# Kernel tuning notes

Measured on AMD Instinct MI355X. Metric: run time of the kernel, lower is better.

Reference implementation:

```python
import jax, jax.numpy as jnp
import numpy as np

HID = 128
NUM_LAYERS = 3
B = 256
ND, ED, SD = 16384, 65536, 131072
NP_, EP, SP = 131072, 524288, 524288


def setup_inputs():
    key = jax.random.key(0)
    ks = jax.random.split(key, 40)
    r = lambda i, sh: jax.random.normal(ks[i], sh, jnp.float32) * 0.05
    ri = lambda i, sh, hi: jax.random.randint(ks[i], sh, 0, hi, jnp.int32)
    return {
        'drug_x': r(0, (ND, 78)),
        'prot_x': r(1, (NP_, 70)),
        'd_feature': r(2, (B, HID)),
        'p_feature': r(3, (B, HID)),
        'drug_edge_index': ri(4, (2, ED), ND),
        'drug_batch': jnp.sort(ri(5, (ND,), B)),
        'drug_sub_node': ri(6, (SD,), ND),
        'drug_sub_ind': ri(7, (SD,), ND),
        'prot_edge_index': ri(8, (2, EP), NP_),
        'prot_batch': jnp.sort(ri(9, (NP_,), B)),
        'prot_sub_node': ri(10, (SP,), NP_),
        'prot_sub_ind': ri(11, (SP,), NP_),
        'enc_Wd': r(12, (78, HID)), 'enc_bd': r(13, (HID,)),
        'enc_Wp': r(14, (70, HID)), 'enc_bp': r(15, (HID,)),
        'convW_d': r(16, (NUM_LAYERS, HID, HID)), 'convb_d': r(17, (NUM_LAYERS, HID)),
        'convW_p': r(18, (NUM_LAYERS, HID, HID)), 'convb_p': r(19, (NUM_LAYERS, HID)),
        'bng_d': jnp.ones((NUM_LAYERS, HID), jnp.float32), 'bnb_d': jnp.zeros((NUM_LAYERS, HID), jnp.float32),
        'bng_p': jnp.ones((NUM_LAYERS, HID), jnp.float32), 'bnb_p': jnp.zeros((NUM_LAYERS, HID), jnp.float32),
        'vn_emb_d': r(20, (HID,)), 'vn_emb_p': r(21, (HID,)),
        'vnW_d': r(22, (NUM_LAYERS - 1, HID, HID)), 'vnb_d': r(23, (NUM_LAYERS - 1, HID)),
        'vnW_p': r(24, (NUM_LAYERS - 1, HID, HID)), 'vnb_p': r(25, (NUM_LAYERS - 1, HID)),
        'mlpd1_W': r(26, (2 * HID, HID)), 'mlpd1_b': r(27, (HID,)),
        'mlpd1_g': jnp.ones((HID,), jnp.float32), 'mlpd1_be': jnp.zeros((HID,), jnp.float32),
        'mlpp1_W': r(28, (2 * HID, HID)), 'mlpp1_b': r(29, (HID,)),
        'mlpp1_g': jnp.ones((HID,), jnp.float32), 'mlpp1_be': jnp.zeros((HID,), jnp.float32),
    }


def _bn(x, g, b):
    # training-mode batch norm (batch statistics)
    m = jnp.mean(x, 0)
    v = jnp.var(x, 0)
    return (x - m) * jax.lax.rsqrt(v + 1e-5) * g + b


def _seg_mean(x, ids, n):
    s = jax.ops.segment_sum(x, ids, num_segments=n)
    c = jax.ops.segment_sum(jnp.ones((x.shape[0],), x.dtype), ids, num_segments=n)
    return s / jnp.maximum(c, 1.0)[:, None]


def _gcn(h, W, b, ei, n):
    # PyG GCNConv: sym-normalized A+I, then linear
    src, dst = ei[0], ei[1]
    hw = h @ W
    deg = jax.ops.segment_sum(jnp.ones((src.shape[0],), h.dtype), dst, num_segments=n) + 1.0
    nrm = jax.lax.rsqrt(deg)
    msg = hw[src] * (nrm[src] * nrm[dst])[:, None]  # [E, HID]
    return jax.ops.segment_sum(msg, dst, num_segments=n) + hw * (nrm * nrm)[:, None] + b


def _forward(fl, ints):
    (drug_x, prot_x, d_feature, p_feature, enc_Wd, enc_bd, enc_Wp, enc_bp,
     convW_d, convb_d, convW_p, convb_p, bng_d, bnb_d, bng_p, bnb_p,
     vn_emb_d, vn_emb_p, vnW_d, vnb_d, vnW_p, vnb_p,
     mlpd1_W, mlpd1_b, mlpd1_g, mlpd1_be, mlpp1_W, mlpp1_b, mlpp1_g, mlpp1_be) = fl
    (d_ei, d_batch, d_sn, d_si, p_ei, p_batch, p_sn, p_si) = ints
    Nd, Npn = drug_x.shape[0], prot_x.shape[0]
    Bn = d_feature.shape[0]
    hd = drug_x @ enc_Wd + enc_bd
    hp = prot_x @ enc_Wp + enc_bp
    # virtual node init: learned embedding + pretrained fingerprint feature
    vx_d = vn_emb_d[None, :] + d_feature  # [B, HID]
    vx_p = vn_emb_p[None, :] + p_feature
    for i in range(NUM_LAYERS):
        # virtual-node broadcast -> GCN -> BN -> ReLU (dropout off / eval)
        hd = _gcn(hd + vx_d[d_batch], convW_d[i], convb_d[i], d_ei, Nd)
        hp = _gcn(hp + vx_p[p_batch], convW_p[i], convb_p[i], p_ei, Npn)
        hd = jax.nn.relu(_bn(hd, bng_d[i], bnb_d[i]))
        hp = jax.nn.relu(_bn(hp, bng_p[i], bnb_p[i]))
        # k-hop subgraph structure extraction (scatter_mean back to nodes)
        hd_struct = _seg_mean(hd[d_sn], d_si, Nd)
        hp_struct = _seg_mean(hp[p_sn], p_si, Npn)
        if i < NUM_LAYERS - 1:
            vx_d = vx_d + jax.nn.relu((jax.ops.segment_sum(hd_struct, d_batch, num_segments=Bn) + vx_d) @ vnW_d[i] + vnb_d[i])
            vx_p = vx_p + jax.nn.relu((jax.ops.segment_sum(hp_struct, p_batch, num_segments=Bn) + vx_p) @ vnW_p[i] + vnb_p[i])
    # cross-modal sync: broadcast pooled drug info onto protein nodes & vice versa
    sync_drug = hp_struct + _seg_mean(hd_struct, d_batch, Bn)[p_batch]  # [Np, HID]
    sync_prot = hd_struct + _seg_mean(hp_struct, p_batch, Bn)[d_batch]  # [Nd, HID]
    final_drug = _bn(jnp.concatenate([_seg_mean(sync_prot, d_batch, Bn), d_feature], 1) @ mlpd1_W + mlpd1_b, mlpd1_g, mlpd1_be)
    final_prot = _bn(jnp.concatenate([_seg_mean(sync_drug, p_batch, Bn), p_feature], 1) @ mlpp1_W + mlpp1_b, mlpp1_g, mlpp1_be)
    return final_drug, final_prot


def reference(drug_x, prot_x, d_feature, p_feature, drug_edge_index, drug_batch,
              drug_sub_node, drug_sub_ind, prot_edge_index, prot_batch,
              prot_sub_node, prot_sub_ind, enc_Wd, enc_bd, enc_Wp, enc_bp,
              convW_d, convb_d, convW_p, convb_p, bng_d, bnb_d, bng_p, bnb_p,
              vn_emb_d, vn_emb_p, vnW_d, vnb_d, vnW_p, vnb_p,
              mlpd1_W, mlpd1_b, mlpd1_g, mlpd1_be, mlpp1_W, mlpp1_b, mlpp1_g, mlpp1_be):
    fl = (drug_x, prot_x, d_feature, p_feature, enc_Wd, enc_bd, enc_Wp, enc_bp,
          convW_d, convb_d, convW_p, convb_p, bng_d, bnb_d, bng_p, bnb_p,
          vn_emb_d, vn_emb_p, vnW_d, vnb_d, vnW_p, vnb_p,
          mlpd1_W, mlpd1_b, mlpd1_g, mlpd1_be, mlpp1_W, mlpp1_b, mlpp1_g, mlpp1_be)
    ints = (drug_edge_index, drug_batch, drug_sub_node, drug_sub_ind,
            prot_edge_index, prot_batch, prot_sub_node, prot_sub_ind)
    return _forward(fl, ints)
```

## Files before the change

### kernel.cpp

```cpp
#include <hip/hip_runtime.h>
#include <cstdint>
#include <cstddef>

#define HID 128
#define HB 1024
#define XB 2048

using bf16x8 = __attribute__((ext_vector_type(8))) short;
using f32x4v = __attribute__((ext_vector_type(4))) float;

static __device__ __forceinline__ unsigned short f2b(float x) {
  unsigned int u = __float_as_uint(x);
  unsigned int r = u + 0x7FFFu + ((u >> 16) & 1u);
  return (unsigned short)(r >> 16);
}
static __device__ __forceinline__ float b2f(unsigned short h) {
  return __uint_as_float(((unsigned int)h) << 16);
}

static __device__ __forceinline__ int lowerb(const int* __restrict__ a, int n, int v) {
  int lo = 0, hi = n;
  while (lo < hi) { int m = (lo + hi) >> 1; if (a[m] < v) lo = m + 1; else hi = m; }
  return lo;
}

__global__ __launch_bounds__(256)
void k_prep1(const int* p_dst, int EP, int* deg_p, const int* d_dst, int ED, int* deg_d,
             const int* p_si, int SP, int* scnt_p, const int* d_si, int SD, int* scnt_d,
             const float* Xd, int Kd, unsigned short* Dhi, unsigned short* Dlo, int totD,
             const float* Xp, int Kp, unsigned short* Phi, unsigned short* Plo, int totP,
             const float* convW_d, const float* convW_p,
             const float* enc_Wd, const float* enc_Wp,
             unsigned short* WhiAll, unsigned short* WloAll,
             const float* emb_d, const float* d_feat, float* vx_d,
             const float* emb_p, const float* p_feat, float* vx_p, int vhalf) {
  const int b = blockIdx.x;
  const int tid = threadIdx.x;
  if (b < 4 * HB) {
    const int seg = b & 3, lb = b >> 2;
    const int stride = HB * 256;
    const int* idx = seg == 0 ? p_dst : seg == 1 ? d_dst : seg == 2 ? p_si : d_si;
    int* cnt = seg == 0 ? deg_p : seg == 1 ? deg_d : seg == 2 ? scnt_p : scnt_d;
    const int n = seg == 0 ? EP : seg == 1 ? ED : seg == 2 ? SP : SD;
    for (int i = lb * 256 + tid; i < n; i += stride) atomicAdd(&cnt[idx[i]], 1);
  } else if (b < 4 * HB + XB) {
    const int lb = b - 4 * HB;
    for (int i = lb * 256 + tid; i < totD + totP; i += XB * 256) {
      if (i < totD) {
        const int node = i >> 7, k = i & 127;
        const float v = (k < Kd) ? Xd[(size_t)node * Kd + k] : 0.f;
        const unsigned short hi = f2b(v);
        Dhi[i] = hi;
        Dlo[i] = f2b(v - b2f(hi));
      } else {
        const int j = i - totD;
        const int node = j >> 7, k = j & 127;
        const float v = (k < Kp) ? Xp[(size_t)node * Kp + k] : 0.f;
        const unsigned short hi = f2b(v);
        Phi[j] = hi;
        Plo[j] = f2b(v - b2f(hi));
      }
    }
  } else if (b < 4 * HB + XB + 256) {
    const int lb = b - (4 * HB + XB);
    const int seg = lb >> 5;
    const float* W;
    int K;
    if (seg < 3) { W = convW_d + (size_t)seg * HID * HID; K = 128; }
    else if (seg < 6) { W = convW_p + (size_t)(seg - 3) * HID * HID; K = 128; }
    else if (seg == 6) { W = enc_Wd; K = 78; }
    else { W = enc_Wp; K = 70; }
    unsigned short* Whi = WhiAll + (size_t)seg * HID * HID;
    unsigned short* Wlo = WloAll + (size_t)seg * HID * HID;
    for (int i = (lb & 31) * 256 + tid; i < HID * HID; i += 32 * 256) {
      const int c = i >> 7, k = i & 127;
      const float v = (k < K) ? W[k * HID + c] : 0.f;
      const unsigned short hi = f2b(v);
      Whi[i] = hi;
      Wlo[i] = f2b(v - b2f(hi));
    }
  } else {
    const int lb = b - (4 * HB + XB + 256);
    for (int i = lb * 256 + tid; i < 2 * vhalf; i += 128 * 256) {
      if (i < vhalf) vx_d[i] = emb_d[i & (HID - 1)] + d_feat[i];
      else { const int j = i - vhalf; vx_p[j] = emb_p[j & (HID - 1)] + p_feat[j]; }
    }
  }
}

__global__ void k_nrm_nb(const int* deg_d, float* nrm_d, int ND,
                         const int* deg_p, float* nrm_p, int NP,
                         const int* d_batch, float* nb_d,
                         const int* p_batch, float* nb_p, int B) {
  const int stride = gridDim.x * blockDim.x;
  const int total = ND + NP + 2 * B;
  for (int i = blockIdx.x * blockDim.x + threadIdx.x; i < total; i += stride) {
    if (i < ND) nrm_d[i] = rsqrtf((float)deg_d[i] + 1.0f);
    else if (i < ND + NP) { const int j = i - ND; nrm_p[j] = rsqrtf((float)deg_p[j] + 1.0f); }
    else if (i < ND + NP + B) {
      const int b = i - ND - NP;
      nb_d[b] = (float)(lowerb(d_batch, ND, b + 1) - lowerb(d_batch, ND, b));
    } else {
      const int b = i - ND - NP - B;
      nb_p[b] = (float)(lowerb(p_batch, NP, b + 1) - lowerb(p_batch, NP, b));
    }
  }
}

__global__ __launch_bounds__(256)
void k_scan1_all(const int* c0, int* r0, int n0, int nb0,
                 const int* c1, int* r1, int n1, int nb1,
                 const int* c2, int* r2, int n2, int nb2,
                 const int* c3, int* r3, int n3, int nb3, int* aux) {
  __shared__ int sh[256];
  int b = blockIdx.x, seg = 0;
  if (b >= nb0) { b -= nb0; seg = 1; }
  if (seg == 1 && b >= nb1) { b -= nb1; seg = 2; }
  if (seg == 2 && b >= nb2) { b -= nb2; seg = 3; }
  const int* cnt = seg == 0 ? c0 : seg == 1 ? c1 : seg == 2 ? c2 : c3;
  int* row = seg == 0 ? r0 : seg == 1 ? r1 : seg == 2 ? r2 : r3;
  const int n = seg == 0 ? n0 : seg == 1 ? n1 : seg == 2 ? n2 : n3;
  const int tid = threadIdx.x;
  const int base = b * 1024 + tid * 4;
  int v0 = base + 0 < n ? cnt[base + 0] : 0;
  int v1 = base + 1 < n ? cnt[base + 1] : 0;
  int v2 = base + 2 < n ? cnt[base + 2] : 0;
  int v3 = base + 3 < n ? cnt[base + 3] : 0;
  const int s = v0 + v1 + v2 + v3;
  sh[tid] = s;
  __syncthreads();
  for (int o = 1; o < 256; o <<= 1) {
    const int t = (tid >= o) ? sh[tid - o] : 0;
    __syncthreads();
    sh[tid] += t;
    __syncthreads();
  }
  int excl = sh[tid] - s;
  if (tid == 255) aux[seg * 256 + b] = sh[255];
  if (base + 0 < n) row[base + 0] = excl; excl += v0;
  if (base + 1 < n) row[base + 1] = excl; excl += v1;
  if (base + 2 < n) row[base + 2] = excl; excl += v2;
  if (base + 3 < n) row[base + 3] = excl;
}

__global__ __launch_bounds__(256)
void k_scan2_all(int* aux, int nb0, int nb1, int nb2, int nb3) {
  __shared__ int sh[256];
  const int seg = blockIdx.x;
  const int nb = seg == 0 ? nb0 : seg == 1 ? nb1 : seg == 2 ? nb2 : nb3;
  int* a = aux + seg * 256;
  const int tid = threadIdx.x;
  const int v = tid < nb ? a[tid] : 0;
  sh[tid] = v;
  __syncthreads();
  for (int o = 1; o < 256; o <<= 1) {
    const int t = (tid >= o) ? sh[tid - o] : 0;
    __syncthreads();
    sh[tid] += t;
    __syncthreads();
  }
  if (tid < nb) a[tid] = sh[tid] - v;
}

__global__ __launch_bounds__(256)
void k_scan3_all(int* r0, int n0, int nb0, int t0, int* r1, int n1, int nb1, int t1,
                 int* r2, int n2, int nb2, int t2, int* r3, int n3, int nb3, int t3,
                 const int* aux) {
  int b = blockIdx.x, seg = 0;
  if (b >= nb0) { b -= nb0; seg = 1; }
  if (seg == 1 && b >= nb1) { b -= nb1; seg = 2; }
  if (seg == 2 && b >= nb2) { b -= nb2; seg = 3; }
  int* row = seg == 0 ? r0 : seg == 1 ? r1 : seg == 2 ? r2 : r3;
  const int n = seg == 0 ? n0 : seg == 1 ? n1 : seg == 2 ? n2 : n3;
  const int total = seg == 0 ? t0 : seg == 1 ? t1 : seg == 2 ? t2 : t3;
  const int add = aux[seg * 256 + b];
  const int base = b * 1024 + threadIdx.x * 4;
  #pragma unroll
  for (int k = 0; k < 4; ++k)
    if (base + k < n) row[base + k] += add;
  if (b == 0 && threadIdx.x == 0) row[n] = total;
}

__global__ void k_fill_all(const int* p_src, const int* p_dst, const int* rowE_p, int* curE_p,
                           int* colE_p, int EP,
                           const int* d_src, const int* d_dst, const int* rowE_d, int* curE_d,
                           int* colE_d, int ED,
                           const int* p_sn, const int* p_si, const int* rowS_p, int* curS_p,
                           int* colS_p, int SP,
                           const int* d_sn, const int* d_si, const int* rowS_d, int* curS_d,
                           int* colS_d, int SD) {
  const int seg = blockIdx.x & 3;
  const int lb = blockIdx.x >> 2;
  const int stride = (gridDim.x >> 2) * blockDim.x;
  const int start = lb * blockDim.x + threadIdx.x;
  if (seg == 0) {
    for (int e = start; e < EP; e += stride) {
      const int d = p_dst[e];
      colE_p[rowE_p[d] + atomicAdd(&curE_p[d], 1)] = p_src[e];
    }
  } else if (seg == 1) {
    for (int e = start; e < ED; e += stride) {
      const int d = d_dst[e];
      colE_d[rowE_d[d] + atomicAdd(&curE_d[d], 1)] = d_src[e];
    }
  } else if (seg == 2) {
    for (int j = start; j < SP; j += stride) {
      const int t = p_si[j];
      colS_p[rowS_p[t] + atomicAdd(&curS_p[t], 1)] = p_sn[j];
    }
  } else {
    for (int j = start; j < SD; j += stride) {
      const int t = d_si[j];
      colS_d[rowS_d[t] + atomicAdd(&curS_d[t], 1)] = d_sn[j];
    }
  }
}

template<bool ENC>
__global__ __launch_bounds__(256, 2)
void k_gemm_both(const unsigned short* __restrict__ Zhi0, const unsigned short* __restrict__ Zlo0,
                 const unsigned short* __restrict__ Whi0, const unsigned short* __restrict__ Wlo0,
                 const float* __restrict__ bias0, float* __restrict__ G0, int nbk0,
                 const unsigned short* __restrict__ Zhi1, const unsigned short* __restrict__ Zlo1,
                 const unsigned short* __restrict__ Whi1, const unsigned short* __restrict__ Wlo1,
                 const float* __restrict__ bias1, float* __restrict__ G1,
                 float* __restrict__ stats_sl) {
  __shared__ unsigned short Bt[128 * 132];
  __shared__ float lstats[256];
  const int bid = blockIdx.x;
  const bool isP = bid >= nbk0;
  const int lb = isP ? bid - nbk0 : bid;
  const unsigned short* Zhi = isP ? Zhi1 : Zhi0;
  const unsigned short* Zlo = isP ? Zlo1 : Zlo0;
  const unsigned short* Wthi = isP ? Whi1 : Whi0;
  const unsigned short* Wtlo = isP ? Wlo1 : Wlo0;
  const float* bias = isP ? bias1 : bias0;
  float* G = isP ? G1 : G0;

  const int tid = threadIdx.x;
  const int w = tid >> 6;
  const int l = tid & 63;
  const int l15 = l & 15;
  const int kb = l >> 4;

  for (int i = tid; i < 128 * 16; i += 256) {
    const int c = i >> 4, k8 = i & 15;
    *(bf16x8*)(&Bt[c * 132 + k8 * 8]) = *(const bf16x8*)(Wthi + (size_t)c * 128 + k8 * 8);
  }
  if constexpr (!ENC) lstats[tid] = 0.f;

  const int rbase = lb * 128 + w * 32 + l15;
  bf16x8 ahi[2][4], alo[2][4];
  #pragma unroll
  for (int rt = 0; rt < 2; ++rt)
    #pragma unroll
    for (int ks = 0; ks < 4; ++ks) {
      ahi[rt][ks] = *(const bf16x8*)(Zhi + (size_t)(rbase + rt * 16) * 128 + ks * 32 + kb * 8);
      alo[rt][ks] = *(const bf16x8*)(Zlo + (size_t)(rbase + rt * 16) * 128 + ks * 32 + kb * 8);
    }

  f32x4v acc[2][8];
  #pragma unroll
  for (int rt = 0; rt < 2; ++rt)
    #pragma unroll
    for (int ct = 0; ct < 8; ++ct)
      acc[rt][ct] = (f32x4v){0.f, 0.f, 0.f, 0.f};

  __syncthreads();
  #pragma unroll
  for (int ks = 0; ks < 4; ++ks) {
    #pragma unroll
    for (int ct = 0; ct < 8; ++ct) {
      const bf16x8 b = *(const bf16x8*)(&Bt[(ct * 16 + l15) * 132 + ks * 32 + kb * 8]);
      acc[0][ct] = __builtin_amdgcn_mfma_f32_16x16x32_bf16(ahi[0][ks], b, acc[0][ct], 0, 0, 0);
      acc[1][ct] = __builtin_amdgcn_mfma_f32_16x16x32_bf16(ahi[1][ks], b, acc[1][ct], 0, 0, 0);
      acc[0][ct] = __builtin_amdgcn_mfma_f32_16x16x32_bf16(alo[0][ks], b, acc[0][ct], 0, 0, 0);
      acc[1][ct] = __builtin_amdgcn_mfma_f32_16x16x32_bf16(alo[1][ks], b, acc[1][ct], 0, 0, 0);
    }
  }
  __syncthreads();

  for (int i = tid; i < 128 * 16; i += 256) {
    const int c = i >> 4, k8 = i & 15;
    *(bf16x8*)(&Bt[c * 132 + k8 * 8]) = *(const bf16x8*)(Wtlo + (size_t)c * 128 + k8 * 8);
  }
  __syncthreads();
  #pragma unroll
  for (int ks = 0; ks < 4; ++ks) {
    #pragma unroll
    for (int ct = 0; ct < 8; ++ct) {
      const bf16x8 b = *(const bf16x8*)(&Bt[(ct * 16 + l15) * 132 + ks * 32 + kb * 8]);
      acc[0][ct] = __builtin_amdgcn_mfma_f32_16x16x32_bf16(ahi[0][ks], b, acc[0][ct], 0, 0, 0);
      acc[1][ct] = __builtin_amdgcn_mfma_f32_16x16x32_bf16(ahi[1][ks], b, acc[1][ct], 0, 0, 0);
    }
  }

  float bb[8];
  if constexpr (ENC) {
    #pragma unroll
    for (int ct = 0; ct < 8; ++ct) bb[ct] = bias[ct * 16 + l15];
  }
  float csum[8], csq[8];
  #pragma unroll
  for (int ct = 0; ct < 8; ++ct) { csum[ct] = 0.f; csq[ct] = 0.f; }
  #pragma unroll
  for (int rt = 0; rt < 2; ++rt) {
    const size_t grow = (size_t)lb * 128 + w * 32 + rt * 16 + (l >> 4) * 4;
    #pragma unroll
    for (int j = 0; j < 4; ++j) {
      float* gr = G + (grow + j) * 128 + l15;
      #pragma unroll
      for (int ct = 0; ct < 8; ++ct) {
        float v = acc[rt][ct][j];
        if constexpr (ENC) v += bb[ct];
        gr[ct * 16] = v;
        if constexpr (!ENC) { csum[ct] += v; csq[ct] += v * v; }
      }
    }
  }
  if constexpr (!ENC) {
    #pragma unroll
    for (int ct = 0; ct < 8; ++ct) {
      csum[ct] += __shfl_xor(csum[ct], 16);
      csum[ct] += __shfl_xor(csum[ct], 32);
      csq[ct] += __shfl_xor(csq[ct], 16);
      csq[ct] += __shfl_xor(csq[ct], 32);
    }
    if (l < 16) {
      #pragma unroll
      for (int ct = 0; ct < 8; ++ct) {
        atomicAdd(&lstats[ct * 16 + l], csum[ct]);
        atomicAdd(&lstats[128 + ct * 16 + l], csq[ct]);
      }
    }
    __syncthreads();
    const int slice = (isP ? 32 : 0) + (lb & 31);
    atomicAdd(&stats_sl[(size_t)slice * 256 + tid], lstats[tid]);
  }
}

__global__ __launch_bounds__(128)
void k_bn_scale_both(float* __restrict__ stats_sl,
                     const float* g0, const float* b0, float invN0, float* scsh0, float* zero0,
                     const float* g1, const float* b1, float invN1, float* scsh1, float* zero1,
                     int zn4) {
  const int seg = blockIdx.x;
  float* base = stats_sl + (size_t)seg * 32 * 256;
  const float* g = seg ? g1 : g0;
  const float* bb = seg ? b1 : b0;
  const float invN = seg ? invN1 : invN0;
  float* scsh = seg ? scsh1 : scsh0;
  float* zero = seg ? zero1 : zero0;
  const int c = threadIdx.x;
  float s = 0.f, ss = 0.f;
  for (int k = 0; k < 32; ++k) {
    s += base[(size_t)k * 256 + c];
    ss += base[(size_t)k * 256 + 128 + c];
    base[(size_t)k * 256 + c] = 0.f;
    base[(size_t)k * 256 + 128 + c] = 0.f;
  }
  const float m = s * invN;
  const float var = ss * invN - m * m;
  const float sc = g[c] * rsqrtf(var + 1e-5f);
  scsh[c] = sc;
  scsh[HID + c] = bb[c] - m * sc;
  const float4 z = {0.f, 0.f, 0.f, 0.f};
  for (int i = c; i < zn4; i += 128) ((float4*)zero)[i] = z;
}

template<bool HASF>
__global__ __launch_bounds__(256)
void k_agg_both(const int* rE0, const int* cE0, const float* G0,
                const float* scsh0, const int* bat0, const float* vx0, const float* nrm0,
                unsigned short* Zhi0, unsigned short* Zlo0, int nbk0,
                const int* rE1, const int* cE1, const float* G1,
                const float* scsh1, const int* bat1, const float* vx1, const float* nrm1,
                unsigned short* Zhi1, unsigned short* Zlo1) {
  const int bid = blockIdx.x;
  const bool isP = bid >= nbk0;
  const int lb = isP ? bid - nbk0 : bid;
  const int* rowp = isP ? rE1 : rE0;
  const int* colp = isP ? cE1 : cE0;
  const float* G = isP ? G1 : G0;
  const float* scsh = isP ? scsh1 : scsh0;
  const int* batch = isP ? bat1 : bat0;
  const float* vx = isP ? vx1 : vx0;
  const float* nrm = isP ? nrm1 : nrm0;
  unsigned short* Zhi = isP ? Zhi1 : Zhi0;
  unsigned short* Zlo = isP ? Zlo1 : Zlo0;

  const int tid = threadIdx.x;
  const int node = lb * 8 + (tid >> 5);
  const int c4 = tid & 31;
  float4 sc, shv;
  if constexpr (HASF) {
    sc = ((const float4*)scsh)[c4];
    shv = ((const float4*)(scsh + HID))[c4];
  }
  auto loadU = [&](int i) -> float4 {
    float4 v = *(const float4*)(G + (size_t)i * HID + c4 * 4);
    if constexpr (HASF) {
      v.x = fmaxf(v.x * sc.x + shv.x, 0.f);
      v.y = fmaxf(v.y * sc.y + shv.y, 0.f);
      v.z = fmaxf(v.z * sc.z + shv.z, 0.f);
      v.w = fmaxf(v.w * sc.w + shv.w, 0.f);
    }
    const float4 u = *(const float4*)(vx + (size_t)batch[i] * HID + c4 * 4);
    v.x += u.x; v.y += u.y; v.z += u.z; v.w += u.w;
    return v;
  };
  const int lo = rowp[node], hi = rowp[node + 1];
  const float nv = nrm[node];
  const float s2 = nv * nv;
  float4 acc = loadU(node);
  acc.x *= s2; acc.y *= s2; acc.z *= s2; acc.w *= s2;
  int e = lo;
  for (; e + 4 <= hi; e += 4) {
    const int i0 = colp[e], i1 = colp[e + 1], i2 = colp[e + 2], i3 = colp[e + 3];
    const float w0 = nrm[i0] * nv, w1 = nrm[i1] * nv, w2 = nrm[i2] * nv, w3 = nrm[i3] * nv;
    const float4 v0 = loadU(i0);
    const float4 v1 = loadU(i1);
    const float4 v2 = loadU(i2);
    const float4 v3 = loadU(i3);
    acc.x += v0.x * w0 + v1.x * w1 + v2.x * w2 + v3.x * w3;
    acc.y += v0.y * w0 + v1.y * w1 + v2.y * w2 + v3.y * w3;
    acc.z += v0.z * w0 + v1.z * w1 + v2.z * w2 + v3.z * w3;
    acc.w += v0.w * w0 + v1.w * w1 + v2.w * w2 + v3.w * w3;
  }
  for (; e < hi; ++e) {
    const int i0 = colp[e];
    const float w = nrm[i0] * nv;
    const float4 v = loadU(i0);
    acc.x += v.x * w; acc.y += v.y * w; acc.z += v.z * w; acc.w += v.w * w;
  }
  ushort4 h, lo4;
  h.x = f2b(acc.x); lo4.x = f2b(acc.x - b2f(h.x));
  h.y = f2b(acc.y); lo4.y = f2b(acc.y - b2f(h.y));
  h.z = f2b(acc.z); lo4.z = f2b(acc.z - b2f(h.z));
  h.w = f2b(acc.w); lo4.w = f2b(acc.w - b2f(h.w));
  *(ushort4*)(Zhi + (size_t)node * HID + c4 * 4) = h;
  *(ushort4*)(Zlo + (size_t)node * HID + c4 * 4) = lo4;
}

__global__ __launch_bounds__(256)
void k_sub_pool_both(const int* rS0, const int* cS0, const float* G0, const float* scsh0,
                     const int* bat0, float* sumS0, int nbk0,
                     const int* rS1, const int* cS1, const float* G1, const float* scsh1,
                     const int* bat1, float* sumS1) {
  __shared__ float sh[8][HID];
  __shared__ int batl[8];
  const int bid = blockIdx.x;
  const bool isP = bid >= nbk0;
  const int lb = isP ? bid - nbk0 : bid;
  const int* rowp = isP ? rS1 : rS0;
  const int* colp = isP ? cS1 : cS0;
  const float* G = isP ? G1 : G0;
  const float* scsh = isP ? scsh1 : scsh0;
  const int* batch = isP ? bat1 : bat0;
  float* sumS = isP ? sumS1 : sumS0;

  const int tid = threadIdx.x;
  const int grp = tid >> 5;
  const int node = lb * 8 + grp;
  const int c4 = tid & 31;
  const float4 sc = ((const float4*)scsh)[c4];
  const float4 shv = ((const float4*)(scsh + HID))[c4];
  const int lo = rowp[node], hi = rowp[node + 1];
  float4 acc = {0.f, 0.f, 0.f, 0.f};
  int e = lo;
  for (; e + 4 <= hi; e += 4) {
    const int i0 = colp[e], i1 = colp[e + 1], i2 = colp[e + 2], i3 = colp[e + 3];
    const float4 v0 = *(const float4*)(G + (size_t)i0 * HID + c4 * 4);
    const float4 v1 = *(const float4*)(G + (size_t)i1 * HID + c4 * 4);
    const float4 v2 = *(const float4*)(G + (size_t)i2 * HID + c4 * 4);
    const float4 v3 = *(const float4*)(G + (size_t)i3 * HID + c4 * 4);
    acc.x += fmaxf(v0.x * sc.x + shv.x, 0.f) + fmaxf(v1.x * sc.x + shv.x, 0.f)
           + fmaxf(v2.x * sc.x + shv.x, 0.f) + fmaxf(v3.x * sc.x + shv.x, 0.f);
    acc.y += fmaxf(v0.y * sc.y + shv.y, 0.f) + fmaxf(v1.y * sc.y + shv.y, 0.f)
           + fmaxf(v2.y * sc.y + shv.y, 0.f) + fmaxf(v3.y * sc.y + shv.y, 0.f);
    acc.z += fmaxf(v0.z * sc.z + shv.z, 0.f) + fmaxf(v1.z * sc.z + shv.z, 0.f)
           + fmaxf(v2.z * sc.z + shv.z, 0.f) + fmaxf(v3.z * sc.z + shv.z, 0.f);
    acc.w += fmaxf(v0.w * sc.w + shv.w, 0.f) + fmaxf(v1.w * sc.w + shv.w, 0.f)
           + fmaxf(v2.w * sc.w + shv.w, 0.f) + fmaxf(v3.w * sc.w + shv.w, 0.f);
  }
  for (; e < hi; ++e) {
    const float4 v = *(const float4*)(G + (size_t)colp[e] * HID + c4 * 4);
    acc.x += fmaxf(v.x * sc.x + shv.x, 0.f);
    acc.y += fmaxf(v.y * sc.y + shv.y, 0.f);
    acc.z += fmaxf(v.z * sc.z + shv.z, 0.f);
    acc.w += fmaxf(v.w * sc.w + shv.w, 0.f);
  }
  const float inv = 1.0f / fmaxf((float)(hi - lo), 1.0f);
  acc.x *= inv; acc.y *= inv; acc.z *= inv; acc.w *= inv;
  ((float4*)&sh[grp][0])[c4] = acc;
  if (tid < 8) batl[tid] = batch[lb * 8 + tid];
  __syncthreads();
  if (tid < HID) {
    int cur = batl[0];
    float a = 0.f;
    #pragma unroll
    for (int g = 0; g < 8; ++g) {
      if (batl[g] != cur) {
        atomicAdd(&sumS[(size_t)cur * HID + tid], a);
        a = 0.f;
        cur = batl[g];
      }
      a += sh[g][tid];
    }
    atomicAdd(&sumS[(size_t)cur * HID + tid], a);
  }
}

__global__ __launch_bounds__(128)
void k_vn_update_both(const float* ps0, float* vx0, const float* W0, const float* b0,
                      const float* ps1, float* vx1, const float* W1, const float* b1, int B) {
  const int gb = blockIdx.x;
  const bool isP = gb >= B;
  const int b = isP ? gb - B : gb;
  const float* pooledSum = isP ? ps1 : ps0;
  float* vx = isP ? vx1 : vx0;
  const float* W = isP ? W1 : W0;
  const float* bias = isP ? b1 : b0;
  const int c = threadIdx.x;
  __shared__ float xin[HID];
  xin[c] = pooledSum[(size_t)b * HID + c] + vx[(size_t)b * HID + c];
  __syncthreads();
  float acc = bias[c];
  #pragma unroll 8
  for (int k = 0; k < HID; k += 4) {
    const float4 x = *(const float4*)&xin[k];
    acc += x.x * W[k * HID + c] + x.y * W[(k + 1) * HID + c]
         + x.z * W[(k + 2) * HID + c] + x.w * W[(k + 3) * HID + c];
  }
  vx[(size_t)b * HID + c] += fmaxf(acc, 0.0f);
}

__global__ __launch_bounds__(128)
void k_final_A(const float* __restrict__ sum_Sd, const float* __restrict__ sum_Sp,
               const float* __restrict__ nb_d, const float* __restrict__ nb_p,
               float* __restrict__ A_d, float* __restrict__ A_p) {
  const int b = blockIdx.x, c = threadIdx.x;
  const float nd = nb_d[b], np_ = nb_p[b];
  const float md = sum_Sd[(size_t)b * HID + c] / fmaxf(nd, 1.f);
  const float mp = sum_Sp[(size_t)b * HID + c] / fmaxf(np_, 1.f);
  A_d[(size_t)b * HID + c] = md + (nd > 0.f ? mp : 0.f);
  A_p[(size_t)b * HID + c] = mp + (np_ > 0.f ? md : 0.f);
}

__global__ __launch_bounds__(128)
void k_final_mlp_both(const float* A0, const float* f0, const float* W0, const float* b0,
                      const float* A1, const float* f1, const float* W1, const float* b1,
                      float* __restrict__ fpre, int B) {
  const int gb = blockIdx.x;
  const bool isP = gb >= B;
  const int b = isP ? gb - B : gb;
  const float* A = isP ? A1 : A0;
  const float* feat = isP ? f1 : f0;
  const float* W = isP ? W1 : W0;
  const float* bias = isP ? b1 : b0;
  const int c = threadIdx.x;
  __shared__ float xin[2 * HID];
  xin[c] = A[(size_t)b * HID + c];
  xin[HID + c] = feat[(size_t)b * HID + c];
  __syncthreads();
  float acc = bias[c];
  #pragma unroll 8
  for (int k = 0; k < 2 * HID; k += 4) {
    const float4 x = *(const float4*)&xin[k];
    acc += x.x * W[k * HID + c] + x.y * W[(k + 1) * HID + c]
         + x.z * W[(k + 2) * HID + c] + x.w * W[(k + 3) * HID + c];
  }
  fpre[(size_t)gb * HID + c] = acc;
}

__global__ __launch_bounds__(256)
void k_bn_stats_both(const float* __restrict__ fpre, float* __restrict__ statsF, int B) {
  __shared__ float sh[2][256];
  const int seg = blockIdx.x >= 128 ? 1 : 0;
  const int lb = blockIdx.x - seg * 128;
  const float* X = fpre + (size_t)seg * B * HID;
  float* stats = statsF + seg * 256;
  const int tid = threadIdx.x;
  const int c = tid & (HID - 1);
  const int half = tid >> 7;
  float s = 0.f, ss = 0.f;
  for (int r = lb * 2 + half; r < B; r += 256) {
    const float v = X[(size_t)r * HID + c];
    s += v; ss += v * v;
  }
  sh[0][tid] = s; sh[1][tid] = ss;
  __syncthreads();
  if (tid < HID) {
    atomicAdd(&stats[c], sh[0][tid] + sh[0][tid + 128]);
    atomicAdd(&stats[HID + c], sh[1][tid] + sh[1][tid + 128]);
  }
}

__global__ void k_bn_apply_both(const float* __restrict__ fpre, float* __restrict__ out,
                                const float* __restrict__ statsF,
                                const float* g0, const float* b0,
                                const float* g1, const float* b1, int B, float invN) {
  const int stride = gridDim.x * blockDim.x;
  const int n4 = 2 * B * 32;
  for (int i = blockIdx.x * blockDim.x + threadIdx.x; i < n4; i += stride) {
    const int seg = i >= B * 32 ? 1 : 0;
    const int c4 = i & 31;
    const float* stats = statsF + seg * 256;
    const float4 m4 = ((const float4*)stats)[c4];
    const float4 q4 = ((const float4*)stats)[32 + c4];
    const float4 g4 = ((const float4*)(seg ? g1 : g0))[c4];
    const float4 b4 = ((const float4*)(seg ? b1 : b0))[c4];
    float4 v = ((const float4*)fpre)[i];
    float m, va;
    m = m4.x * invN; va = q4.x * invN - m * m; v.x = (v.x - m) * rsqrtf(va + 1e-5f) * g4.x + b4.x;
    m = m4.y * invN; va = q4.y * invN - m * m; v.y = (v.y - m) * rsqrtf(va + 1e-5f) * g4.y + b4.y;
    m = m4.z * invN; va = q4.z * invN - m * m; v.z = (v.z - m) * rsqrtf(va + 1e-5f) * g4.z + b4.z;
    m = m4.w * invN; va = q4.w * invN - m * m; v.w = (v.w - m) * rsqrtf(va + 1e-5f) * g4.w + b4.w;
    ((float4*)out)[i] = v;
  }
}

extern "C" void kernel_launch(void* const* d_in, const int* in_sizes, int n_in,
                              void* d_out, int out_size, void* d_ws, size_t ws_size,
                              hipStream_t stream) {
  const float* drug_x   = (const float*)d_in[0];
  const float* prot_x   = (const float*)d_in[1];
  const float* d_feat   = (const float*)d_in[2];
  const float* p_feat   = (const float*)d_in[3];
  const int*   d_ei     = (const int*)d_in[4];
  const int*   d_batch  = (const int*)d_in[5];
  const int*   d_sn     = (const int*)d_in[6];
  const int*   d_si     = (const int*)d_in[7];
  const int*   p_ei     = (const int*)d_in[8];
  const int*   p_batch  = (const int*)d_in[9];
  const int*   p_sn     = (const int*)d_in[10];
  const int*   p_si     = (const int*)d_in[11];
  const float* enc_Wd   = (const float*)d_in[12];
  const float* enc_bd   = (const float*)d_in[13];
  const float* enc_Wp   = (const float*)d_in[14];
  const float* enc_bp   = (const float*)d_in[15];
  const float* convW_d  = (const float*)d_in[16];
  const float* convW_p  = (const float*)d_in[18];
  const float* bng_d    = (const float*)d_in[20];
  const float* bnb_d    = (const float*)d_in[21];
  const float* bng_p    = (const float*)d_in[22];
  const float* bnb_p    = (const float*)d_in[23];
  const float* vn_emb_d = (const float*)d_in[24];
  const float* vn_emb_p = (const float*)d_in[25];
  const float* vnW_d    = (const float*)d_in[26];
  const float* vnb_d    = (const float*)d_in[27];
  const float* vnW_p    = (const float*)d_in[28];
  const float* vnb_p    = (const float*)d_in[29];
  const float* mlpd1_W  = (const float*)d_in[30];
  const float* mlpd1_b  = (const float*)d_in[31];
  const float* mlpd1_g  = (const float*)d_in[32];
  const float* mlpd1_be = (const float*)d_in[33];
  const float* mlpp1_W  = (const float*)d_in[34];
  const float* mlpp1_b  = (const float*)d_in[35];
  const float* mlpp1_g  = (const float*)d_in[36];
  const float* mlpp1_be = (const float*)d_in[37];

  const int ND = in_sizes[5];
  const int ED = in_sizes[4] / 2;
  const int SD = in_sizes[6];
  const int NP = in_sizes[9];
  const int EP = in_sizes[8] / 2;
  const int SP = in_sizes[10];
  const int B  = in_sizes[2] / HID;
  (void)n_in; (void)out_size; (void)ws_size;

  char* wsb = (char*)d_ws;
  size_t off = 0;
  auto alloc = [&](size_t bytes) -> void* {
    void* p = (void*)(wsb + off);
    off = (off + bytes + 255) & ~(size_t)255;
    return p;
  };
  float* Gp = (float*)alloc((size_t)NP * HID * 4);
  unsigned short* Zhi_p = (unsigned short*)alloc((size_t)NP * HID * 2);
  unsigned short* Zlo_p = (unsigned short*)alloc((size_t)NP * HID * 2);
  float* Gd = (float*)alloc((size_t)ND * HID * 4);
  unsigned short* Zhi_d = (unsigned short*)alloc((size_t)ND * HID * 2);
  unsigned short* Zlo_d = (unsigned short*)alloc((size_t)ND * HID * 2);
  unsigned short* WhiAll = (unsigned short*)alloc((size_t)8 * HID * HID * 2);
  unsigned short* WloAll = (unsigned short*)alloc((size_t)8 * HID * HID * 2);
  float* nrm_p = (float*)alloc((size_t)NP * 4);
  float* nrm_d = (float*)alloc((size_t)ND * 4);
  int* rowE_p = (int*)alloc((size_t)(NP + 1) * 4);
  int* rowE_d = (int*)alloc((size_t)(ND + 1) * 4);
  int* rowS_p = (int*)alloc((size_t)(NP + 1) * 4);
  int* rowS_d = (int*)alloc((size_t)(ND + 1) * 4);
  int* colE_p = (int*)alloc((size_t)EP * 4);
  int* colE_d = (int*)alloc((size_t)ED * 4);
  int* colS_p = (int*)alloc((size_t)SP * 4);
  int* colS_d = (int*)alloc((size_t)SD * 4);
  int* aux    = (int*)alloc(4 * 256 * 4);
  float* vx_d  = (float*)alloc((size_t)B * HID * 4);
  float* vx_p  = (float*)alloc((size_t)B * HID * 4);
  float* sum_Sd = (float*)alloc((size_t)B * HID * 4);
  float* sum_Sp = (float*)alloc((size_t)B * HID * 4);
  float* A_d   = (float*)alloc((size_t)B * HID * 4);
  float* A_p   = (float*)alloc((size_t)B * HID * 4);
  float* nb_d  = (float*)alloc((size_t)B * 4);
  float* nb_p  = (float*)alloc((size_t)B * 4);
  float* scsh_d = (float*)alloc(2 * HID * 4);
  float* scsh_p = (float*)alloc(2 * HID * 4);
  float* fpre  = (float*)alloc((size_t)2 * B * HID * 4);
  float* statsF = (float*)alloc(2 * 256 * 4);
  const size_t zstart = off;
  int* deg_p  = (int*)alloc((size_t)NP * 4);
  int* deg_d  = (int*)alloc((size_t)ND * 4);
  int* scnt_p = (int*)alloc((size_t)NP * 4);
  int* scnt_d = (int*)alloc((size_t)ND * 4);
  int* curE_p = (int*)alloc((size_t)NP * 4);
  int* curE_d = (int*)alloc((size_t)ND * 4);
  int* curS_p = (int*)alloc((size_t)NP * 4);
  int* curS_d = (int*)alloc((size_t)ND * 4);
  float* stats_sl = (float*)alloc((size_t)64 * 256 * 4);
  const size_t zend = off;

  const int* d_src = d_ei;  const int* d_dst = d_ei + ED;
  const int* p_src = p_ei;  const int* p_dst = p_ei + EP;

  hipMemsetAsync(wsb + zstart, 0, zend - zstart, stream);
  k_prep1<<<4 * HB + XB + 256 + 128, 256, 0, stream>>>(
      p_dst, EP, deg_p, d_dst, ED, deg_d, p_si, SP, scnt_p, d_si, SD, scnt_d,
      drug_x, 78, Zhi_d, Zlo_d, ND * HID, prot_x, 70, Zhi_p, Zlo_p, NP * HID,
      convW_d, convW_p, enc_Wd, enc_Wp, WhiAll, WloAll,
      vn_emb_d, d_feat, vx_d, vn_emb_p, p_feat, vx_p, B * HID);
  k_nrm_nb<<<1024, 256, 0, stream>>>(deg_d, nrm_d, ND, deg_p, nrm_p, NP,
                                     d_batch, nb_d, p_batch, nb_p, B);
  const int nbP = (NP + 1023) / 1024, nbD = (ND + 1023) / 1024;
  k_scan1_all<<<2 * nbP + 2 * nbD, 256, 0, stream>>>(
      deg_p, rowE_p, NP, nbP, deg_d, rowE_d, ND, nbD,
      scnt_p, rowS_p, NP, nbP, scnt_d, rowS_d, ND, nbD, aux);
  k_scan2_all<<<4, 256, 0, stream>>>(aux, nbP, nbD, nbP, nbD);
  k_scan3_all<<<2 * nbP + 2 * nbD, 256, 0, stream>>>(
      rowE_p, NP, nbP, EP, rowE_d, ND, nbD, ED,
      rowS_p, NP, nbP, SP, rowS_d, ND, nbD, SD, aux);
  k_fill_all<<<4096, 256, 0, stream>>>(
      p_src, p_dst, rowE_p, curE_p, colE_p, EP,
      d_src, d_dst, rowE_d, curE_d, colE_d, ED,
      p_sn, p_si, rowS_p, curS_p, colS_p, SP,
      d_sn, d_si, rowS_d, curS_d, colS_d, SD);

  k_gemm_both<true><<<ND / 128 + NP / 128, 256, 0, stream>>>(
      Zhi_d, Zlo_d, WhiAll + (size_t)6 * HID * HID, WloAll + (size_t)6 * HID * HID,
      enc_bd, Gd, ND / 128,
      Zhi_p, Zlo_p, WhiAll + (size_t)7 * HID * HID, WloAll + (size_t)7 * HID * HID,
      enc_bp, Gp, nullptr);

  for (int l = 0; l < 3; ++l) {
    if (l == 0)
      k_agg_both<false><<<ND / 8 + NP / 8, 256, 0, stream>>>(
          rowE_d, colE_d, Gd, nullptr, d_batch, vx_d, nrm_d, Zhi_d, Zlo_d, ND / 8,
          rowE_p, colE_p, Gp, nullptr, p_batch, vx_p, nrm_p, Zhi_p, Zlo_p);
    else
      k_agg_both<true><<<ND / 8 + NP / 8, 256, 0, stream>>>(
          rowE_d, colE_d, Gd, scsh_d, d_batch, vx_d, nrm_d, Zhi_d, Zlo_d, ND / 8,
          rowE_p, colE_p, Gp, scsh_p, p_batch, vx_p, nrm_p, Zhi_p, Zlo_p);
    k_gemm_both<false><<<ND / 128 + NP / 128, 256, 0, stream>>>(
        Zhi_d, Zlo_d, WhiAll + (size_t)l * HID * HID, WloAll + (size_t)l * HID * HID,
        nullptr, Gd, ND / 128,
        Zhi_p, Zlo_p, WhiAll + (size_t)(3 + l) * HID * HID, WloAll + (size_t)(3 + l) * HID * HID,
        nullptr, Gp, stats_sl);
    k_bn_scale_both<<<2, 128, 0, stream>>>(stats_sl,
        bng_d + l * HID, bnb_d + l * HID, 1.0f / (float)ND, scsh_d, sum_Sd,
        bng_p + l * HID, bnb_p + l * HID, 1.0f / (float)NP, scsh_p, sum_Sp,
        B * HID / 4);
    k_sub_pool_both<<<ND / 8 + NP / 8, 256, 0, stream>>>(
        rowS_d, colS_d, Gd, scsh_d, d_batch, sum_Sd, ND / 8,
        rowS_p, colS_p, Gp, scsh_p, p_batch, sum_Sp);
    if (l < 2)
      k_vn_update_both<<<2 * B, 128, 0, stream>>>(
          sum_Sd, vx_d, vnW_d + (size_t)l * HID * HID, vnb_d + l * HID,
          sum_Sp, vx_p, vnW_p + (size_t)l * HID * HID, vnb_p + l * HID, B);
  }

  k_final_A<<<B, 128, 0, stream>>>(sum_Sd, sum_Sp, nb_d, nb_p, A_d, A_p);
  k_final_mlp_both<<<2 * B, 128, 0, stream>>>(A_d, d_feat, mlpd1_W, mlpd1_b,
                                              A_p, p_feat, mlpp1_W, mlpp1_b, fpre, B);
  hipMemsetAsync(statsF, 0, 2 * 256 * 4, stream);
  k_bn_stats_both<<<256, 256, 0, stream>>>(fpre, statsF, B);
  k_bn_apply_both<<<128, 256, 0, stream>>>(fpre, (float*)d_out, statsF,
                                           mlpd1_g, mlpd1_be, mlpp1_g, mlpp1_be,
                                           B, 1.0f / (float)B);
}
```

Measured before the change: 709.1 us.

## Store GEMM outputs as bf16 and fuse encoder GEMM with CSR fill

The intermediate G buffers written by the GEMM and gathered by the aggregation and subgraph-pool kernels are stored as bf16 instead of fp32. This halves the bytes of the scattered gathers, but BN statistics are still computed from the fp32 accumulators, so consumers now see rounded values. Separately, the encoder GEMM and the CSR fill kernel are merged into one launch so their independent work can overlap. The merged kernel reserves the GEMM shared memory in every block, including the fill blocks.

New measurement: 720.7 us. No clear change (+1.6%).

```diff
diff --git a/kernel.cpp b/kernel.cpp
--- a/kernel.cpp
+++ b/kernel.cpp
@@ -16,6 +16,9 @@
 }
 static __device__ __forceinline__ float b2f(unsigned short h) {
   return __uint_as_float(((unsigned int)h) << 16);
+}
+static __device__ __forceinline__ float4 b2f4(ushort4 h) {
+  return make_float4(b2f(h.x), b2f(h.y), b2f(h.z), b2f(h.w));
 }
 
 static __device__ __forceinline__ int lowerb(const int* __restrict__ a, int n, int v) {
@@ -181,63 +184,13 @@
   if (b == 0 && threadIdx.x == 0) row[n] = total;
 }
 
-__global__ void k_fill_all(const int* p_src, const int* p_dst, const int* rowE_p, int* curE_p,
-                           int* colE_p, int EP,
-                           const int* d_src, const int* d_dst, const int* rowE_d, int* curE_d,
-                           int* colE_d, int ED,
-                           const int* p_sn, const int* p_si, const int* rowS_p, int* curS_p,
-                           int* colS_p, int SP,
-                           const int* d_sn, const int* d_si, const int* rowS_d, int* curS_d,
-                           int* colS_d, int SD) {
-  const int seg = blockIdx.x & 3;
-  const int lb = blockIdx.x >> 2;
-  const int stride = (gridDim.x >> 2) * blockDim.x;
-  const int start = lb * blockDim.x + threadIdx.x;
-  if (seg == 0) {
-    for (int e = start; e < EP; e += stride) {
-      const int d = p_dst[e];
-      colE_p[rowE_p[d] + atomicAdd(&curE_p[d], 1)] = p_src[e];
-    }
-  } else if (seg == 1) {
-    for (int e = start; e < ED; e += stride) {
-      const int d = d_dst[e];
-      colE_d[rowE_d[d] + atomicAdd(&curE_d[d], 1)] = d_src[e];
-    }
-  } else if (seg == 2) {
-    for (int j = start; j < SP; j += stride) {
-      const int t = p_si[j];
-      colS_p[rowS_p[t] + atomicAdd(&curS_p[t], 1)] = p_sn[j];
-    }
-  } else {
-    for (int j = start; j < SD; j += stride) {
-      const int t = d_si[j];
-      colS_d[rowS_d[t] + atomicAdd(&curS_d[t], 1)] = d_sn[j];
-    }
-  }
-}
-
 template<bool ENC>
-__global__ __launch_bounds__(256, 2)
-void k_gemm_both(const unsigned short* __restrict__ Zhi0, const unsigned short* __restrict__ Zlo0,
-                 const unsigned short* __restrict__ Whi0, const unsigned short* __restrict__ Wlo0,
-                 const float* __restrict__ bias0, float* __restrict__ G0, int nbk0,
-                 const unsigned short* __restrict__ Zhi1, const unsigned short* __restrict__ Zlo1,
-                 const unsigned short* __restrict__ Whi1, const unsigned short* __restrict__ Wlo1,
-                 const float* __restrict__ bias1, float* __restrict__ G1,
-                 float* __restrict__ stats_sl) {
-  __shared__ unsigned short Bt[128 * 132];
-  __shared__ float lstats[256];
-  const int bid = blockIdx.x;
-  const bool isP = bid >= nbk0;
-  const int lb = isP ? bid - nbk0 : bid;
-  const unsigned short* Zhi = isP ? Zhi1 : Zhi0;
-  const unsigned short* Zlo = isP ? Zlo1 : Zlo0;
-  const unsigned short* Wthi = isP ? Whi1 : Whi0;
-  const unsigned short* Wtlo = isP ? Wlo1 : Wlo0;
-  const float* bias = isP ? bias1 : bias0;
-  float* G = isP ? G1 : G0;
-
-  const int tid = threadIdx.x;
+static __device__ __forceinline__
+void gemm_block(unsigned short* __restrict__ Bt, float* __restrict__ lstats, int lb, int tid,
+                const unsigned short* __restrict__ Zhi, const unsigned short* __restrict__ Zlo,
+                const unsigned short* __restrict__ Wthi, const unsigned short* __restrict__ Wtlo,
+                const float* __restrict__ bias, unsigned short* __restrict__ G,
+                float* __restrict__ stats_sl, int slice) {
   const int w = tid >> 6;
   const int l = tid & 63;
   const int l15 = l & 15;
@@ -308,12 +261,12 @@
     const size_t grow = (size_t)lb * 128 + w * 32 + rt * 16 + (l >> 4) * 4;
     #pragma unroll
     for (int j = 0; j < 4; ++j) {
-      float* gr = G + (grow + j) * 128 + l15;
+      unsigned short* gr = G + (grow + j) * 128 + l15;
       #pragma unroll
       for (int ct = 0; ct < 8; ++ct) {
         float v = acc[rt][ct][j];
         if constexpr (ENC) v += bb[ct];
-        gr[ct * 16] = v;
+        gr[ct * 16] = f2b(v);
         if constexpr (!ENC) { csum[ct] += v; csq[ct] += v * v; }
       }
     }
@@ -334,8 +287,79 @@
       }
     }
     __syncthreads();
-    const int slice = (isP ? 32 : 0) + (lb & 31);
     atomicAdd(&stats_sl[(size_t)slice * 256 + tid], lstats[tid]);
+  }
+}
+
+__global__ __launch_bounds__(256, 2)
+void k_gemm_both(const unsigned short* Zhi0, const unsigned short* Zlo0,
+                 const unsigned short* Whi0, const unsigned short* Wlo0,
+                 unsigned short* G0, int nbk0,
+                 const unsigned short* Zhi1, const unsigned short* Zlo1,
+                 const unsigned short* Whi1, const unsigned short* Wlo1,
+                 unsigned short* G1, float* stats_sl) {
+  __shared__ unsigned short Bt[128 * 132];
+  __shared__ float lstats[256];
+  const int bid = blockIdx.x;
+  const bool isP = bid >= nbk0;
+  const int lb = isP ? bid - nbk0 : bid;
+  gemm_block<false>(Bt, lstats, lb, threadIdx.x,
+                    isP ? Zhi1 : Zhi0, isP ? Zlo1 : Zlo0,
+                    isP ? Whi1 : Whi0, isP ? Wlo1 : Wlo0,
+                    nullptr, isP ? G1 : G0, stats_sl, (isP ? 32 : 0) + (lb & 31));
+}
+
+__global__ __launch_bounds__(256, 2)
+void k_fill_enc(const unsigned short* Zhi0, const unsigned short* Zlo0,
+                const unsigned short* Whi0, const unsigned short* Wlo0,
+                const float* bias0, unsigned short* G0, int nG0,
+                const unsigned short* Zhi1, const unsigned short* Zlo1,
+                const unsigned short* Whi1, const unsigned short* Wlo1,
+                const float* bias1, unsigned short* G1, int nG1,
+                const int* p_src, const int* p_dst, const int* rowE_p, int* curE_p,
+                int* colE_p, int EP,
+                const int* d_src, const int* d_dst, const int* rowE_d, int* curE_d,
+                int* colE_d, int ED,
+                const int* p_sn, const int* p_si, const int* rowS_p, int* curS_p,
+                int* colS_p, int SP,
+                const int* d_sn, const int* d_si, const int* rowS_d, int* curS_d,
+                int* colS_d, int SD) {
+  __shared__ unsigned short Bt[128 * 132];
+  __shared__ float lstats[256];
+  const int b = blockIdx.x;
+  if (b < nG0 + nG1) {
+    const bool isP = b >= nG0;
+    gemm_block<true>(Bt, lstats, isP ? b - nG0 : b, threadIdx.x,
+                     isP ? Zhi1 : Zhi0, isP ? Zlo1 : Zlo0,
+                     isP ? Whi1 : Whi0, isP ? Wlo1 : Wlo0,
+                     isP ? bias1 : bias0, isP ? G1 : G0, nullptr, 0);
+    return;
+  }
+  const int fb = b - nG0 - nG1;
+  const int seg = fb & 3;
+  const int lb = fb >> 2;
+  const int stride = 1024 * 256;
+  const int start = lb * 256 + threadIdx.x;
+  if (seg == 0) {
+    for (int e = start; e < EP; e += stride) {
+      const int d = p_dst[e];
+      colE_p[rowE_p[d] + atomicAdd(&curE_p[d], 1)] = p_src[e];
+    }
+  } else if (seg == 1) {
+    for (int e = start; e < ED; e += stride) {
+      const int d = d_dst[e];
+      colE_d[rowE_d[d] + atomicAdd(&curE_d[d], 1)] = d_src[e];
+    }
+  } else if (seg == 2) {
+    for (int j = start; j < SP; j += stride) {
+      const int t = p_si[j];
+      colS_p[rowS_p[t] + atomicAdd(&curS_p[t], 1)] = p_sn[j];
+    }
+  } else {
+    for (int j = start; j < SD; j += stride) {
+      const int t = d_si[j];
+      colS_d[rowS_d[t] + atomicAdd(&curS_d[t], 1)] = d_sn[j];
+    }
   }
 }
 
@@ -370,10 +394,10 @@
 
 template<bool HASF>
 __global__ __launch_bounds__(256)
-void k_agg_both(const int* rE0, const int* cE0, const float* G0,
+void k_agg_both(const int* rE0, const int* cE0, const unsigned short* G0,
                 const float* scsh0, const int* bat0, const float* vx0, const float* nrm0,
                 unsigned short* Zhi0, unsigned short* Zlo0, int nbk0,
-                const int* rE1, const int* cE1, const float* G1,
+                const int* rE1, const int* cE1, const unsigned short* G1,
                 const float* scsh1, const int* bat1, const float* vx1, const float* nrm1,
                 unsigned short* Zhi1, unsigned short* Zlo1) {
   const int bid = blockIdx.x;
@@ -381,7 +405,7 @@
   const int lb = isP ? bid - nbk0 : bid;
   const int* rowp = isP ? rE1 : rE0;
   const int* colp = isP ? cE1 : cE0;
-  const float* G = isP ? G1 : G0;
+  const unsigned short* G = isP ? G1 : G0;
   const float* scsh = isP ? scsh1 : scsh0;
   const int* batch = isP ? bat1 : bat0;
   const float* vx = isP ? vx1 : vx0;
@@ -398,7 +422,7 @@
     shv = ((const float4*)(scsh + HID))[c4];
   }
   auto loadU = [&](int i) -> float4 {
-    float4 v = *(const float4*)(G + (size_t)i * HID + c4 * 4);
+    float4 v = b2f4(*(const ushort4*)(G + (size_t)i * HID + c4 * 4));
     if constexpr (HASF) {
       v.x = fmaxf(v.x * sc.x + shv.x, 0.f);
       v.y = fmaxf(v.y * sc.y + shv.y, 0.f);
@@ -443,9 +467,9 @@
 }
 
 __global__ __launch_bounds__(256)
-void k_sub_pool_both(const int* rS0, const int* cS0, const float* G0, const float* scsh0,
+void k_sub_pool_both(const int* rS0, const int* cS0, const unsigned short* G0, const float* scsh0,
                      const int* bat0, float* sumS0, int nbk0,
-                     const int* rS1, const int* cS1, const float* G1, const float* scsh1,
+                     const int* rS1, const int* cS1, const unsigned short* G1, const float* scsh1,
                      const int* bat1, float* sumS1) {
   __shared__ float sh[8][HID];
   __shared__ int batl[8];
@@ -454,7 +478,7 @@
   const int lb = isP ? bid - nbk0 : bid;
   const int* rowp = isP ? rS1 : rS0;
   const int* colp = isP ? cS1 : cS0;
-  const float* G = isP ? G1 : G0;
+  const unsigned short* G = isP ? G1 : G0;
   const float* scsh = isP ? scsh1 : scsh0;
   const int* batch = isP ? bat1 : bat0;
   float* sumS = isP ? sumS1 : sumS0;
@@ -470,10 +494,10 @@
   int e = lo;
   for (; e + 4 <= hi; e += 4) {
     const int i0 = colp[e], i1 = colp[e + 1], i2 = colp[e + 2], i3 = colp[e + 3];
-    const float4 v0 = *(const float4*)(G + (size_t)i0 * HID + c4 * 4);
-    const float4 v1 = *(const float4*)(G + (size_t)i1 * HID + c4 * 4);
-    const float4 v2 = *(const float4*)(G + (size_t)i2 * HID + c4 * 4);
-    const float4 v3 = *(const float4*)(G + (size_t)i3 * HID + c4 * 4);
+    const float4 v0 = b2f4(*(const ushort4*)(G + (size_t)i0 * HID + c4 * 4));
+    const float4 v1 = b2f4(*(const ushort4*)(G + (size_t)i1 * HID + c4 * 4));
+    const float4 v2 = b2f4(*(const ushort4*)(G + (size_t)i2 * HID + c4 * 4));
+    const float4 v3 = b2f4(*(const ushort4*)(G + (size_t)i3 * HID + c4 * 4));
     acc.x += fmaxf(v0.x * sc.x + shv.x, 0.f) + fmaxf(v1.x * sc.x + shv.x, 0.f)
            + fmaxf(v2.x * sc.x + shv.x, 0.f) + fmaxf(v3.x * sc.x + shv.x, 0.f);
     acc.y += fmaxf(v0.y * sc.y + shv.y, 0.f) + fmaxf(v1.y * sc.y + shv.y, 0.f)
@@ -484,7 +508,7 @@
            + fmaxf(v2.w * sc.w + shv.w, 0.f) + fmaxf(v3.w * sc.w + shv.w, 0.f);
   }
   for (; e < hi; ++e) {
-    const float4 v = *(const float4*)(G + (size_t)colp[e] * HID + c4 * 4);
+    const float4 v = b2f4(*(const ushort4*)(G + (size_t)colp[e] * HID + c4 * 4));
     acc.x += fmaxf(v.x * sc.x + shv.x, 0.f);
     acc.y += fmaxf(v.y * sc.y + shv.y, 0.f);
     acc.z += fmaxf(v.z * sc.z + shv.z, 0.f);
@@ -676,10 +700,10 @@
     off = (off + bytes + 255) & ~(size_t)255;
     return p;
   };
-  float* Gp = (float*)alloc((size_t)NP * HID * 4);
+  unsigned short* Gp = (unsigned short*)alloc((size_t)NP * HID * 2);
   unsigned short* Zhi_p = (unsigned short*)alloc((size_t)NP * HID * 2);
   unsigned short* Zlo_p = (unsigned short*)alloc((size_t)NP * HID * 2);
-  float* Gd = (float*)alloc((size_t)ND * HID * 4);
+  unsigned short* Gd = (unsigned short*)alloc((size_t)ND * HID * 2);
   unsigned short* Zhi_d = (unsigned short*)alloc((size_t)ND * HID * 2);
   unsigned short* Zlo_d = (unsigned short*)alloc((size_t)ND * HID * 2);
   unsigned short* WhiAll = (unsigned short*)alloc((size_t)8 * HID * HID * 2);
@@ -738,17 +762,17 @@
   k_scan3_all<<<2 * nbP + 2 * nbD, 256, 0, stream>>>(
       rowE_p, NP, nbP, EP, rowE_d, ND, nbD, ED,
       rowS_p, NP, nbP, SP, rowS_d, ND, nbD, SD, aux);
-  k_fill_all<<<4096, 256, 0, stream>>>(
+
+  const int nG0 = ND / 128, nG1 = NP / 128;
+  k_fill_enc<<<nG0 + nG1 + 4096, 256, 0, stream>>>(
+      Zhi_d, Zlo_d, WhiAll + (size_t)6 * HID * HID, WloAll + (size_t)6 * HID * HID,
+      enc_bd, Gd, nG0,
+      Zhi_p, Zlo_p, WhiAll + (size_t)7 * HID * HID, WloAll + (size_t)7 * HID * HID,
+      enc_bp, Gp, nG1,
       p_src, p_dst, rowE_p, curE_p, colE_p, EP,
       d_src, d_dst, rowE_d, curE_d, colE_d, ED,
       p_sn, p_si, rowS_p, curS_p, colS_p, SP,
       d_sn, d_si, rowS_d, curS_d, colS_d, SD);
-
-  k_gemm_both<true><<<ND / 128 + NP / 128, 256, 0, stream>>>(
-      Zhi_d, Zlo_d, WhiAll + (size_t)6 * HID * HID, WloAll + (size_t)6 * HID * HID,
-      enc_bd, Gd, ND / 128,
-      Zhi_p, Zlo_p, WhiAll + (size_t)7 * HID * HID, WloAll + (size_t)7 * HID * HID,
-      enc_bp, Gp, nullptr);
 
   for (int l = 0; l < 3; ++l) {
     if (l == 0)
@@ -759,11 +783,11 @@
       k_agg_both<true><<<ND / 8 + NP / 8, 256, 0, stream>>>(
           rowE_d, colE_d, Gd, scsh_d, d_batch, vx_d, nrm_d, Zhi_d, Zlo_d, ND / 8,
           rowE_p, colE_p, Gp, scsh_p, p_batch, vx_p, nrm_p, Zhi_p, Zlo_p);
-    k_gemm_both<false><<<ND / 128 + NP / 128, 256, 0, stream>>>(
+    k_gemm_both<<<ND / 128 + NP / 128, 256, 0, stream>>>(
         Zhi_d, Zlo_d, WhiAll + (size_t)l * HID * HID, WloAll + (size_t)l * HID * HID,
-        nullptr, Gd, ND / 128,
+        Gd, ND / 128,
         Zhi_p, Zlo_p, WhiAll + (size_t)(3 + l) * HID * HID, WloAll + (size_t)(3 + l) * HID * HID,
-        nullptr, Gp, stats_sl);
+        Gp, stats_sl);
     k_bn_scale_both<<<2, 128, 0, stream>>>(stats_sl,
         bng_d + l * HID, bnb_d + l * HID, 1.0f / (float)ND, scsh_d, sum_Sd,
         bng_p + l * HID, bnb_p + l * HID, 1.0f / (float)NP, scsh_p, sum_Sp,
```
